# Kernel tuning notes

Measured on AMD Instinct MI355X. Metric: run time of the kernel, lower is better.

Reference implementation:

```python
import jax, jax.numpy as jnp
import numpy as np

B, N, K, D, F, H = 8, 512, 16, 256, 1024, 8


def _ln(x, g, b):
    m = jnp.mean(x, axis=-1, keepdims=True)
    v = jnp.var(x, axis=-1, keepdims=True)
    return (x - m) / jnp.sqrt(v + 1e-5) * g + b


def _mlp(x, W1, b1, W2, b2):
    return jax.nn.gelu(x @ W1 + b1, approximate=False) @ W2 + b2


def setup_inputs() -> dict:
    key = jax.random.key(0)
    ks = jax.random.split(key, 16)
    s = 0.02
    inp = {
        'x': jax.random.normal(ks[0], (N, B, D), jnp.float32),
        'e': jax.random.normal(ks[1], (B, N, K, D), jnp.float32),
        'edge_index': jax.random.randint(ks[2], (B, N, K), 0, N),
        'Wq': jax.random.normal(ks[3], (D, D), jnp.float32) * s,
        'bq': jnp.zeros((D,), jnp.float32),
        'Wk': jax.random.normal(ks[4], (D, D), jnp.float32) * s,
        'bk': jnp.zeros((D,), jnp.float32),
        'Wv': jax.random.normal(ks[5], (D, D), jnp.float32) * s,
        'bv': jnp.zeros((D,), jnp.float32),
        'Wo': jax.random.normal(ks[6], (D, D), jnp.float32) * s,
        'bo': jnp.zeros((D,), jnp.float32),
        'nW1': jax.random.normal(ks[7], (D, F), jnp.float32) * s,
        'nb1': jnp.zeros((F,), jnp.float32),
        'nW2': jax.random.normal(ks[8], (F, D), jnp.float32) * s,
        'nb2': jnp.zeros((D,), jnp.float32),
        'eW1': jax.random.normal(ks[9], (D, F), jnp.float32) * s,
        'eb1': jnp.zeros((F,), jnp.float32),
        'eW2': jax.random.normal(ks[10], (F, D), jnp.float32) * s,
        'eb2': jnp.zeros((D,), jnp.float32),
        'na_g': jnp.ones((D,), jnp.float32), 'na_b': jnp.zeros((D,), jnp.float32),
        'ea_g': jnp.ones((D,), jnp.float32), 'ea_b': jnp.zeros((D,), jnp.float32),
        'nf_g': jnp.ones((D,), jnp.float32), 'nf_b': jnp.zeros((D,), jnp.float32),
        'ef_g': jnp.ones((D,), jnp.float32), 'ef_b': jnp.zeros((D,), jnp.float32),
    }
    return inp


def reference(x, e, edge_index, Wq, bq, Wk, bk, Wv, bv, Wo, bo,
              nW1, nb1, nW2, nb2, eW1, eb1, eW2, eb2,
              na_g, na_b, ea_g, ea_b, nf_g, nf_b, ef_g, ef_b):
    n, b, d = x.shape
    hd = d // H
    xt = jnp.transpose(x, (1, 0, 2))  # (B, N, D) residual in batch-first layout
    bi = jnp.arange(b)[:, None, None]
    ni = jnp.arange(n)[None, :, None]

    # scatter edge features into dense additive attention bias (B, N, N)
    attn_bias = jnp.zeros((b, n, n), x.dtype).at[bi, ni, edge_index].set(e.mean(-1))

    def heads(t):  # (B,N,D) -> (B,H,N,hd)
        return t.reshape(b, n, H, hd).transpose(0, 2, 1, 3)

    q = heads(xt @ Wq + bq) * (hd ** -0.5)
    k = heads(xt @ Wk + bk)
    v = heads(xt @ Wv + bv)
    logits = jnp.einsum('bhnd,bhmd->bhnm', q, k) + attn_bias[:, None]
    attn = jax.nn.softmax(logits, axis=-1)  # (B,H,N,N)
    out = jnp.einsum('bhnm,bhmd->bhnd', attn, v)
    out = out.transpose(0, 2, 1, 3).reshape(b, n, d) @ Wo + bo

    xn = _ln(xt + out, na_g, na_b)  # (B,N,D)

    # edge update: gather attn weights and neighbor node features via edge_index
    weights = attn.mean(axis=1)  # (B,N,N) head-averaged
    w = weights[bi, edge_index, ni]  # (B,N,K): weights[b, edge_index[b,n,k], n]
    gathered = xt[jnp.arange(b)[:, None, None], edge_index]  # (B,N,K,D)
    e2 = _ln(e + w[..., None] * gathered, ea_g, ea_b)

    xn = _ln(xn + _mlp(xn, nW1, nb1, nW2, nb2), nf_g, nf_b)
    e2 = _ln(e2 + _mlp(e2, eW1, eb1, eW2, eb2), ef_g, ef_b)
    return jnp.transpose(xn, (1, 0, 2)), e2
```

## Files before the change

### kernel.cpp

```cpp
#include <hip/hip_runtime.h>
#include <hip/hip_bf16.h>
#include <hip/hip_fp8.h>
#include <math.h>

#define B_ 8
#define N_ 512
#define K_ 16
#define D_ 256
#define F_ 1024
#define H_ 8
#define HD_ 32
#define M_ (B_*N_)
#define R_ (B_*N_*K_)

typedef __bf16 bf16x8 __attribute__((ext_vector_type(8)));
typedef float  f32x4  __attribute__((ext_vector_type(4)));
typedef long   i64x2  __attribute__((ext_vector_type(2)));

__device__ inline short bf16s(float f) {
    __hip_bfloat16 h = __float2bfloat16(f);
    return *reinterpret_cast<short*>(&h);
}
__device__ inline float b2f(short s) {
    union { float f; unsigned u; } v; v.u = ((unsigned)(unsigned short)s) << 16; return v.f;
}
__device__ inline unsigned char f8e4m3(float f) {
    union { __hip_fp8_e4m3 h; unsigned char c; } u;
    u.h = __hip_fp8_e4m3(f);
    return u.c;
}
__device__ __forceinline__ float gelu_f(float x) {
    const float z = fabsf(x) * 0.70710678118654752f;
    const float t = __builtin_amdgcn_rcpf(1.f + 0.3275911f*z);
    const float p = t*(0.254829592f + t*(-0.284496736f + t*(1.421413741f
                  + t*(-1.453152027f + t*1.061405429f))));
    float er = 1.f - p*__expf(-z*z);
    er = (x >= 0.f) ? er : -er;
    return 0.5f*x*(1.f + er);
}
__device__ __forceinline__ int f8pos(int w, int row) {
    return ((((w >> 3) & 3) ^ (row & 3)) << 4) | ((w >> 5) << 3) | (w & 7);
}
__device__ __forceinline__ int hperm(int k) {
    return (k & ~63) | ((k & 15) << 2) | ((k >> 4) & 3);
}

__device__ __forceinline__ void gload16(const void* g, void* l) {
    __builtin_amdgcn_global_load_lds(
        (const __attribute__((address_space(1))) unsigned int*)g,
        (__attribute__((address_space(3))) unsigned int*)l, 16, 0, 0);
}

__global__ __launch_bounds__(256) void transposeAll(
        const float* __restrict__ Wq, const float* __restrict__ Wk,
        const float* __restrict__ Wv, const float* __restrict__ Wo,
        const float* __restrict__ nW1, const float* __restrict__ nW2,
        const float* __restrict__ eW1, const float* __restrict__ eW2,
        short* __restrict__ WqkvT, short* __restrict__ WoT,
        short* __restrict__ nW1T, short* __restrict__ nW2T,
        short* __restrict__ eW1T, unsigned char* __restrict__ eW2T8)
{
    const float* W; short* WT = nullptr; int Kk, Nn; float sc = 1.f;
    switch (blockIdx.z) {
        case 0: W=Wq;  WT=WqkvT;          Kk=256;  Nn=256;  sc=0.17677669529663687f; break;
        case 1: W=Wk;  WT=WqkvT+256*256;  Kk=256;  Nn=256;  break;
        case 2: W=Wv;  WT=WqkvT+512*256;  Kk=256;  Nn=256;  break;
        case 3: W=Wo;  WT=WoT;            Kk=256;  Nn=256;  break;
        case 4: W=nW1; WT=nW1T;           Kk=256;  Nn=1024; break;
        case 5: W=nW2; WT=nW2T;           Kk=1024; Nn=256;  break;
        case 6: W=eW1; WT=eW1T;           Kk=256;  Nn=1024; break;
        default:W=eW2;                    Kk=1024; Nn=256;  break;
    }
    const int bx = blockIdx.x, by = blockIdx.y;
    if (bx >= Nn/32 || by >= Kk/32) return;
    __shared__ float tile[32][33];
    int tx = threadIdx.x & 31, ty = threadIdx.x >> 5;
    #pragma unroll
    for (int j = 0; j < 4; ++j) {
        int k = by*32 + ty + j*8;
        tile[ty + j*8][tx] = W[(size_t)k*Nn + bx*32 + tx];
    }
    __syncthreads();
    if (blockIdx.z == 7) {
        #pragma unroll
        for (int j = 0; j < 4; ++j) {
            int n = bx*32 + ty + j*8;
            int kp = hperm(by*32 + tx);
            eW2T8[(size_t)n*1024 + (kp & ~63) + f8pos(kp & 63, n)] =
                f8e4m3(tile[tx][ty + j*8] * 64.f);
        }
    } else if (blockIdx.z == 5) {
        #pragma unroll
        for (int j = 0; j < 4; ++j) {
            int n = bx*32 + ty + j*8;
            WT[(size_t)n*1024 + hperm(by*32 + tx)] = bf16s(tile[tx][ty + j*8]);
        }
    } else {
        #pragma unroll
        for (int j = 0; j < 4; ++j) {
            int n = bx*32 + ty + j*8;
            WT[(size_t)n*Kk + by*32 + tx] = bf16s(tile[tx][ty + j*8] * sc);
        }
    }
}

__global__ __launch_bounds__(256) void build_bqkv(const float* __restrict__ bq,
        const float* __restrict__ bk, const float* __restrict__ bv,
        float* __restrict__ bqkv)
{
    int t = blockIdx.x*256 + threadIdx.x;
    if (t >= 768) return;
    float v = (t < 256) ? bq[t]*0.17677669529663687f
            : (t < 512) ? bk[t-256] : bv[t-512];
    bqkv[t] = v;
}

__global__ __launch_bounds__(256) void conv_x(const float* __restrict__ x,
        short* __restrict__ xtb)
{
    int row = blockIdx.x;
    int d = threadIdx.x;
    int b = row >> 9, n = row & 511;
    xtb[(size_t)row*D_ + d] = bf16s(x[((size_t)n*B_ + b)*D_ + d]);
}

__global__ __launch_bounds__(256) void edge_means(const float* __restrict__ e,
        float* __restrict__ means)
{
    long row = (long)blockIdx.x*4 + (threadIdx.x >> 6);
    int lane = threadIdx.x & 63;
    float4 v = ((const float4*)(e + row*D_))[lane];
    float s = v.x + v.y + v.z + v.w;
    for (int o = 1; o < 64; o <<= 1) s += __shfl_xor(s, o);
    if (lane == 0) means[row] = s * (1.f/D_);
}

__global__ __launch_bounds__(256) void bias_build(const int* __restrict__ ei,
        const float* __restrict__ means, float* __restrict__ biasb)
{
    const int r0 = blockIdx.x * 16;
    float4* bp4 = (float4*)(biasb + (size_t)r0*N_);
    #pragma unroll
    for (int i = threadIdx.x; i < 16*N_/4; i += 256)
        bp4[i] = make_float4(0.f, 0.f, 0.f, 0.f);
    __syncthreads();
    if (threadIdx.x < 16) {
        const int idx = r0 + threadIdx.x;
        const int* ep = ei + (size_t)idx*K_;
        const float* mp = means + (size_t)idx*K_;
        float* bp = biasb + (size_t)idx*N_;
        for (int k = 0; k < K_; ++k) bp[ep[k]] = mp[k];
    }
}

__global__ __launch_bounds__(256) void gemm_qkv(
        const short* __restrict__ A, const short* __restrict__ BT,
        const float* __restrict__ bias, short* __restrict__ Cb,
        short* __restrict__ vtb, int Kk)
{
    __shared__ __align__(16) short As[128*32];
    __shared__ __align__(16) short Bs[128*32];
    const int t = threadIdx.x;
    const int lane = t & 63;
    const int wave = t >> 6;
    const int wr = (wave >> 1) * 64;
    const int wc = (wave & 1) * 64;
    const int bm = blockIdx.x, bn = blockIdx.y;
    f32x4 acc[4][4] = {};
    const int srow = lane >> 2;
    const int sk   = (lane & 3) * 8;
    const int fr = lane & 15;
    const int fk = (lane >> 4) * 8;
    for (int k0 = 0; k0 < Kk; k0 += 32) {
        __syncthreads();
        #pragma unroll
        for (int i = 0; i < 2; ++i) {
            const int rb = wave*16 + i*64;
            gload16(A  + (size_t)(bm*128 + rb + srow)*Kk + k0 + sk, &As[rb*32]);
            gload16(BT + (size_t)(bn*128 + rb + srow)*Kk + k0 + sk, &Bs[rb*32]);
        }
        __syncthreads();
        bf16x8 af[4], bfr[4];
        #pragma unroll
        for (int i2 = 0; i2 < 4; ++i2)
            af[i2] = *(const bf16x8*)&As[(wr + i2*16 + fr)*32 + fk];
        #pragma unroll
        for (int n2 = 0; n2 < 4; ++n2)
            bfr[n2] = *(const bf16x8*)&Bs[(wc + n2*16 + fr)*32 + fk];
        #pragma unroll
        for (int i2 = 0; i2 < 4; ++i2)
            #pragma unroll
            for (int n2 = 0; n2 < 4; ++n2)
                acc[i2][n2] = __builtin_amdgcn_mfma_f32_16x16x32_bf16(
                        af[i2], bfr[n2], acc[i2][n2], 0, 0, 0);
    }
    const int fq4 = (lane >> 4) * 4;
    #pragma unroll
    for (int i2 = 0; i2 < 4; ++i2) {
        #pragma unroll
        for (int n2 = 0; n2 < 4; ++n2) {
            const int col = bn*128 + wc + n2*16 + fr;
            const float bv = bias[col];
            const int rowb = bm*128 + wr + i2*16 + fq4;
            if (col < 512) {
                #pragma unroll
                for (int r2 = 0; r2 < 4; ++r2)
                    Cb[(size_t)(rowb + r2)*512 + col] = bf16s(acc[i2][n2][r2] + bv);
            } else {
                const int b = rowb >> 9, n = rowb & 511;
                const int dv = col - 512, h = dv >> 5, dh = dv & 31;
                short4 s4;
                s4.x = bf16s(acc[i2][n2][0] + bv);
                s4.y = bf16s(acc[i2][n2][1] + bv);
                s4.z = bf16s(acc[i2][n2][2] + bv);
                s4.w = bf16s(acc[i2][n2][3] + bv);
                *(short4*)&vtb[((size_t)((b*H_ + h)*HD_ + dh))*512 + n] = s4;
            }
        }
    }
}

__global__ __launch_bounds__(512, 4) void gemm_gelu_f8(
        const short* __restrict__ A, const short* __restrict__ BT,
        const float* __restrict__ bias, unsigned char* __restrict__ C8, int Kk)
{
    __shared__ __align__(16) short As[2][128*32];
    __shared__ __align__(16) short Bs[2][256*32];
    const int t = threadIdx.x;
    const int lane = t & 63;
    const int wave = t >> 6;
    const int wrg = (wave >> 2) * 64;
    const int wc  = (wave & 3) * 64;
    const int bm = blockIdx.x, bn = blockIdx.y;
    f32x4 acc[4][4] = {};
    const int srow = lane >> 2;
    const int sk   = (lane & 3) * 8;
    const int fr = lane & 15;
    const int fk = (lane >> 4) * 8;
    auto stage = [&](int s, int k0) {
        {
            const int rb = wave*16;
            gload16(A + (size_t)(bm*128 + rb + srow)*Kk + k0 + sk, &As[s][rb*32]);
        }
        #pragma unroll
        for (int i = 0; i < 2; ++i) {
            const int rb = wave*16 + i*128;
            gload16(BT + (size_t)(bn*256 + rb + srow)*Kk + k0 + sk, &Bs[s][rb*32]);
        }
    };
    stage(0, 0);
    __syncthreads();
    int cur = 0;
    for (int k0 = 0; k0 < Kk; k0 += 32) {
        if (k0 + 32 < Kk) stage(cur ^ 1, k0 + 32);
        bf16x8 af[4], bfr[4];
        #pragma unroll
        for (int i2 = 0; i2 < 4; ++i2)
            af[i2] = *(const bf16x8*)&As[cur][(wrg + i2*16 + fr)*32 + fk];
        #pragma unroll
        for (int n2 = 0; n2 < 4; ++n2)
            bfr[n2] = *(const bf16x8*)&Bs[cur][(wc + n2*16 + fr)*32 + fk];
        #pragma unroll
        for (int i2 = 0; i2 < 4; ++i2)
            #pragma unroll
            for (int n2 = 0; n2 < 4; ++n2)
                acc[i2][n2] = __builtin_amdgcn_mfma_f32_16x16x32_bf16(
                        af[i2], bfr[n2], acc[i2][n2], 0, 0, 0);
        __syncthreads();
        cur ^= 1;
    }
    const int fq4 = (lane >> 4) * 4;
    const int chunk = (bn*4 + (wc >> 6)) * 64;
    #pragma unroll
    for (int i2 = 0; i2 < 4; ++i2) {
        #pragma unroll
        for (int r2 = 0; r2 < 4; ++r2) {
            const int row = bm*128 + wrg + i2*16 + fq4 + r2;
            float v[4];
            #pragma unroll
            for (int n2 = 0; n2 < 4; ++n2)
                v[n2] = gelu_f(acc[i2][n2][r2] + bias[bn*256 + wc + n2*16 + fr]);
            int word = __builtin_amdgcn_cvt_pk_fp8_f32(v[0]*16.f, v[1]*16.f, 0, false);
            word = __builtin_amdgcn_cvt_pk_fp8_f32(v[2]*16.f, v[3]*16.f, word, true);
            *(unsigned int*)(C8 + (size_t)row*1024 + chunk + f8pos(fr*4, row))
                = (unsigned int)word;
        }
    }
}

template<int MODE>
__global__ __launch_bounds__(256, 3) void gemm64(
        const short* __restrict__ A, const short* __restrict__ BT,
        const float* __restrict__ bias, const float* __restrict__ resf,
        const float* __restrict__ g, const float* __restrict__ bt,
        float* __restrict__ out, short* __restrict__ outb, int Kk)
{
    __shared__ __align__(16) short As[2][64*32];
    __shared__ __align__(16) short Bs[2][256*32];
    __shared__ float rs[64][4][2];
    __shared__ float mr[64][2];
    const int t = threadIdx.x;
    const int lane = t & 63;
    const int wave = t >> 6;
    const int wc = wave * 64;
    const int bm = blockIdx.x;
    const int Bbase = (MODE == 0) ? blockIdx.y * 256 : 0;
    f32x4 acc[4][4] = {};
    const int srow = lane >> 2;
    const int sk   = (lane & 3) * 8;
    const int fr = lane & 15;
    const int fk = (lane >> 4) * 8;
    auto stage = [&](int s, int k0) {
        {
            const int rb = wave*16;
            gload16(A + (size_t)(bm*64 + rb + srow)*Kk + k0 + sk, &As[s][rb*32]);
        }
        #pragma unroll
        for (int i = 0; i < 4; ++i) {
            const int rb = wave*16 + i*64;
            gload16(BT + (size_t)(Bbase + rb + srow)*Kk + k0 + sk, &Bs[s][rb*32]);
        }
    };
    stage(0, 0);
    __syncthreads();
    int cur = 0;
    for (int k0 = 0; k0 < Kk; k0 += 32) {
        if (k0 + 32 < Kk) stage(cur ^ 1, k0 + 32);
        bf16x8 af[4], bfr[4];
        #pragma unroll
        for (int i2 = 0; i2 < 4; ++i2)
            af[i2] = *(const bf16x8*)&As[cur][(i2*16 + fr)*32 + fk];
        #pragma unroll
        for (int n2 = 0; n2 < 4; ++n2)
            bfr[n2] = *(const bf16x8*)&Bs[cur][(wc + n2*16 + fr)*32 + fk];
        #pragma unroll
        for (int i2 = 0; i2 < 4; ++i2)
            #pragma unroll
            for (int n2 = 0; n2 < 4; ++n2)
                acc[i2][n2] = __builtin_amdgcn_mfma_f32_16x16x32_bf16(
                        af[i2], bfr[n2], acc[i2][n2], 0, 0, 0);
        __syncthreads();
        cur ^= 1;
    }
    const int fq4 = (lane >> 4) * 4;
    if constexpr (MODE == 0) {
        const int chunk = (blockIdx.y*4 + (wc >> 6)) * 64;
        #pragma unroll
        for (int i2 = 0; i2 < 4; ++i2) {
            #pragma unroll
            for (int r2 = 0; r2 < 4; ++r2) {
                const int row = bm*64 + i2*16 + fq4 + r2;
                float v[4];
                #pragma unroll
                for (int n2 = 0; n2 < 4; ++n2)
                    v[n2] = gelu_f(acc[i2][n2][r2]
                                   + bias[blockIdx.y*256 + wc + n2*16 + fr]);
                short4 s4;
                s4.x = bf16s(v[0]); s4.y = bf16s(v[1]);
                s4.z = bf16s(v[2]); s4.w = bf16s(v[3]);
                *(short4*)&outb[(size_t)row*1024 + chunk + fr*4] = s4;
            }
        }
        return;
    }
    float ps[4][4] = {}, pq[4][4] = {};
    #pragma unroll
    for (int i2 = 0; i2 < 4; ++i2) {
        #pragma unroll
        for (int n2 = 0; n2 < 4; ++n2) {
            const int c = wc + n2*16 + fr;
            const float bv = bias[c];
            #pragma unroll
            for (int r2 = 0; r2 < 4; ++r2) {
                const int row = i2*16 + fq4 + r2;
                const size_t grow = (size_t)bm*64 + row;
                float rv;
                if constexpr (MODE == 1) {
                    const int bb = (int)(grow >> 9), nn = (int)(grow & 511);
                    rv = resf[((size_t)nn*B_ + bb)*256 + c];
                } else {
                    rv = resf[grow*256 + c];
                }
                float v = acc[i2][n2][r2] + bv + rv;
                acc[i2][n2][r2] = v;
                ps[i2][r2] += v;
                pq[i2][r2] += v*v;
            }
        }
    }
    #pragma unroll
    for (int i2 = 0; i2 < 4; ++i2)
        #pragma unroll
        for (int r2 = 0; r2 < 4; ++r2)
            #pragma unroll
            for (int o = 1; o < 16; o <<= 1) {
                ps[i2][r2] += __shfl_xor(ps[i2][r2], o);
                pq[i2][r2] += __shfl_xor(pq[i2][r2], o);
            }
    if ((lane & 15) == 0) {
        #pragma unroll
        for (int i2 = 0; i2 < 4; ++i2)
            #pragma unroll
            for (int r2 = 0; r2 < 4; ++r2) {
                const int row = i2*16 + fq4 + r2;
                rs[row][wave][0] = ps[i2][r2];
                rs[row][wave][1] = pq[i2][r2];
            }
    }
    __syncthreads();
    if (t < 64) {
        float S = 0.f, Q = 0.f;
        #pragma unroll
        for (int w = 0; w < 4; ++w) { S += rs[t][w][0]; Q += rs[t][w][1]; }
        const float mean = S * (1.f/D_);
        mr[t][0] = mean;
        mr[t][1] = rsqrtf(Q * (1.f/D_) - mean*mean + 1e-5f);
    }
    __syncthreads();
    #pragma unroll
    for (int i2 = 0; i2 < 4; ++i2) {
        #pragma unroll
        for (int n2 = 0; n2 < 4; ++n2) {
            const int c = wc + n2*16 + fr;
            const float gv = g[c], bv2 = bt[c];
            #pragma unroll
            for (int r2 = 0; r2 < 4; ++r2) {
                const int row = i2*16 + fq4 + r2;
                const size_t grow = (size_t)bm*64 + row;
                const float o = (acc[i2][n2][r2] - mr[row][0])*mr[row][1]*gv + bv2;
                if constexpr (MODE == 1) {
                    out[grow*256 + c] = o;
                    outb[grow*256 + c] = bf16s(o);
                } else {
                    const int bb = (int)(grow >> 9), nn = (int)(grow & 511);
                    out[((size_t)nn*B_ + bb)*D_ + c] = o;
                }
            }
        }
    }
}

__global__ __launch_bounds__(512, 4) void gemm_ln2f8(
        const unsigned char* __restrict__ A, const unsigned char* __restrict__ BT,
        const float* __restrict__ bias, const short* __restrict__ resb,
        const float* __restrict__ g, const float* __restrict__ bt,
        float* __restrict__ out)
{
    __shared__ __align__(16) unsigned char As[2][128*64];
    __shared__ __align__(16) unsigned char Bs[2][256*64];
    __shared__ float rs[128][4][2];
    __shared__ float mr[128][2];
    const int t = threadIdx.x;
    const int lane = t & 63;
    const int wave = t >> 6;
    const int wrg = (wave >> 2) * 64;
    const int wc  = (wave & 3) * 64;
    const int bm = blockIdx.x;
    f32x4 acc[4][4] = {};
    const int srow = lane >> 2;
    const int skb  = (lane & 3) * 16;
    const int fr = lane & 15;
    const int q16 = (lane >> 4);
    auto stage = [&](int s, int k0) {
        {
            const int rb = wave*16;
            gload16(A + (size_t)(bm*128 + rb + srow)*1024 + k0 + skb, &As[s][rb*64]);
        }
        #pragma unroll
        for (int i = 0; i < 2; ++i) {
            const int rb = wave*16 + i*128;
            gload16(BT + (size_t)(rb + srow)*1024 + k0 + skb, &Bs[s][rb*64]);
        }
    };
    stage(0, 0);
    __syncthreads();
    int cur = 0;
    for (int k0 = 0; k0 < 1024; k0 += 64) {
        if (k0 + 64 < 1024) stage(cur ^ 1, k0 + 64);
        long a8[2][4], b8[2][4];
        #pragma unroll
        for (int i2 = 0; i2 < 4; ++i2) {
            const int ar = wrg + i2*16 + fr;
            const i64x2 av = *(const i64x2*)&As[cur][ar*64 + ((q16 ^ (ar & 3)) << 4)];
            a8[0][i2] = av[0]; a8[1][i2] = av[1];
        }
        #pragma unroll
        for (int n2 = 0; n2 < 4; ++n2) {
            const int br = wc + n2*16 + fr;
            const i64x2 bv = *(const i64x2*)&Bs[cur][br*64 + ((q16 ^ (br & 3)) << 4)];
            b8[0][n2] = bv[0]; b8[1][n2] = bv[1];
        }
        #pragma unroll
        for (int s = 0; s < 2; ++s)
            #pragma unroll
            for (int i2 = 0; i2 < 4; ++i2)
                #pragma unroll
                for (int n2 = 0; n2 < 4; ++n2)
                    acc[i2][n2] = __builtin_amdgcn_mfma_f32_16x16x32_fp8_fp8(
                            a8[s][i2], b8[s][n2], acc[i2][n2], 0, 0, 0);
        __syncthreads();
        cur ^= 1;
    }
    const int fq4 = (lane >> 4) * 4;
    float ps[4][4] = {}, pq[4][4] = {};
    #pragma unroll
    for (int i2 = 0; i2 < 4; ++i2) {
        #pragma unroll
        for (int n2 = 0; n2 < 4; ++n2) {
            const int c = wc + n2*16 + fr;
            const float bv = bias[c];
            #pragma unroll
            for (int r2 = 0; r2 < 4; ++r2) {
                const int row = wrg + i2*16 + fq4 + r2;
                const size_t grow = (size_t)bm*128 + row;
                float v = acc[i2][n2][r2]*(1.f/1024.f) + bv + b2f(resb[grow*256 + c]);
                acc[i2][n2][r2] = v;
                ps[i2][r2] += v;
                pq[i2][r2] += v*v;
            }
        }
    }
    #pragma unroll
    for (int i2 = 0; i2 < 4; ++i2)
        #pragma unroll
        for (int r2 = 0; r2 < 4; ++r2)
            #pragma unroll
            for (int o = 1; o < 16; o <<= 1) {
                ps[i2][r2] += __shfl_xor(ps[i2][r2], o);
                pq[i2][r2] += __shfl_xor(pq[i2][r2], o);
            }
    if ((lane & 15) == 0) {
        #pragma unroll
        for (int i2 = 0; i2 < 4; ++i2)
            #pragma unroll
            for (int r2 = 0; r2 < 4; ++r2) {
                const int row = wrg + i2*16 + fq4 + r2;
                rs[row][wave & 3][0] = ps[i2][r2];
                rs[row][wave & 3][1] = pq[i2][r2];
            }
    }
    __syncthreads();
    if (t < 128) {
        float S = 0.f, Q = 0.f;
        #pragma unroll
        for (int w = 0; w < 4; ++w) { S += rs[t][w][0]; Q += rs[t][w][1]; }
        const float mean = S * (1.f/D_);
        mr[t][0] = mean;
        mr[t][1] = rsqrtf(Q * (1.f/D_) - mean*mean + 1e-5f);
    }
    __syncthreads();
    #pragma unroll
    for (int i2 = 0; i2 < 4; ++i2) {
        #pragma unroll
        for (int n2 = 0; n2 < 4; ++n2) {
            const int c = wc + n2*16 + fr;
            const float gv = g[c], bv2 = bt[c];
            #pragma unroll
            for (int r2 = 0; r2 < 4; ++r2) {
                const int row = wrg + i2*16 + fq4 + r2;
                const size_t grow = (size_t)bm*128 + row;
                out[grow*256 + c] = (acc[i2][n2][r2] - mr[row][0])*mr[row][1]*gv + bv2;
            }
        }
    }
}

__global__ __launch_bounds__(256) void attn_fused(const short* __restrict__ qkb,
        const short* __restrict__ vtb, const float* __restrict__ biasb,
        float* __restrict__ rowsum, short* __restrict__ actx)
{
    __shared__ __align__(16) short Qs[128*32];
    __shared__ __align__(16) short Ks[128*32];
    __shared__ __align__(16) short Vs[32*128];
    __shared__ __align__(16) short Ps[128*128];
    const int it = blockIdx.x, bh = blockIdx.y;
    const int b = bh >> 3, h = bh & 7;
    const int t = threadIdx.x;
    const int lane = t & 63;
    const int wave = t >> 6;
    const int wr0 = wave * 32;
    const int srow = lane >> 2;
    const int sk   = (lane & 3) * 8;
    const int srow8 = lane >> 4;
    const int ck16  = lane & 15;
    const int fr = lane & 15;
    const int fk = (lane >> 4) * 8;
    const int fq4 = (lane >> 4) * 4;
    const int I0 = it * 128;
    #pragma unroll
    for (int i = 0; i < 2; ++i) {
        const int rb = wave*16 + i*64;
        gload16(qkb + (size_t)(b*N_ + I0 + rb + srow)*512 + h*HD_ + sk, &Qs[rb*32]);
    }
    float rsum[2][4] = {};
    f32x4 apv[2][2] = {};
    const float LOG2E = 1.4426950408889634f;
    for (int jt = 0; jt < 4; ++jt) {
        const int J0 = jt * 128;
        __syncthreads();
        #pragma unroll
        for (int i = 0; i < 2; ++i) {
            const int rb = wave*16 + i*64;
            gload16(qkb + (size_t)(b*N_ + J0 + rb + srow)*512 + 256 + h*HD_ + sk, &Ks[rb*32]);
        }
        #pragma unroll
        for (int i = 0; i < 2; ++i) {
            const int db = wave*8 + i*4;
            const int dh = db + srow8;
            gload16(vtb + ((size_t)bh*HD_ + dh)*512 + J0 + ((ck16 ^ (dh & 7)) * 8),
                    &Vs[db*128]);
        }
        __syncthreads();
        bf16x8 aq[2], kf8[8];
        #pragma unroll
        for (int i2 = 0; i2 < 2; ++i2)
            aq[i2] = *(const bf16x8*)&Qs[(wr0 + i2*16 + fr)*32 + fk];
        #pragma unroll
        for (int n2 = 0; n2 < 8; ++n2)
            kf8[n2] = *(const bf16x8*)&Ks[(n2*16 + fr)*32 + fk];
        #pragma unroll
        for (int i2 = 0; i2 < 2; ++i2) {
            #pragma unroll
            for (int n2 = 0; n2 < 8; ++n2) {
                f32x4 z = {0.f, 0.f, 0.f, 0.f};
                f32x4 s = __builtin_amdgcn_mfma_f32_16x16x32_bf16(aq[i2], kf8[n2], z, 0, 0, 0);
                const int jg = J0 + n2*16 + fr;
                #pragma unroll
                for (int r2 = 0; r2 < 4; ++r2) {
                    const int rloc = wr0 + i2*16 + fq4 + r2;
                    const float l = s[r2] + biasb[((size_t)b*N_ + I0 + rloc)*N_ + jg];
                    const float p = exp2f(fminf(l, 80.f) * LOG2E);
                    rsum[i2][r2] += p;
                    int idx = rloc*128 + n2*16 + fr;
                    idx ^= (rloc & 7) << 3;
                    Ps[idx] = bf16s(p);
                }
            }
        }
        __syncthreads();
        #pragma unroll
        for (int ks = 0; ks < 4; ++ks) {
            bf16x8 ap[2], bv[2];
            #pragma unroll
            for (int i2 = 0; i2 < 2; ++i2) {
                const int r = wr0 + i2*16 + fr;
                int idx = r*128 + ks*32 + fk;
                idx ^= (r & 7) << 3;
                ap[i2] = *(const bf16x8*)&Ps[idx];
            }
            #pragma unroll
            for (int n2 = 0; n2 < 2; ++n2) {
                const int dh = n2*16 + fr;
                const int q = lane >> 4;
                const int slot = (ks*4 + q) ^ (dh & 7);
                bv[n2] = *(const bf16x8*)&Vs[dh*128 + slot*8];
            }
            #pragma unroll
            for (int i2 = 0; i2 < 2; ++i2)
                #pragma unroll
                for (int n2 = 0; n2 < 2; ++n2)
                    apv[i2][n2] = __builtin_amdgcn_mfma_f32_16x16x32_bf16(
                            ap[i2], bv[n2], apv[i2][n2], 0, 0, 0);
        }
    }
    #pragma unroll
    for (int i2 = 0; i2 < 2; ++i2)
        #pragma unroll
        for (int r2 = 0; r2 < 4; ++r2)
            #pragma unroll
            for (int o = 1; o < 16; o <<= 1)
                rsum[i2][r2] += __shfl_xor(rsum[i2][r2], o);
    #pragma unroll
    for (int i2 = 0; i2 < 2; ++i2) {
        #pragma unroll
        for (int r2 = 0; r2 < 4; ++r2) {
            const int row = wr0 + i2*16 + fq4 + r2;
            if (fr == 0)
                rowsum[(size_t)bh*N_ + I0 + row] = rsum[i2][r2];
            const float inv = 1.f / rsum[i2][r2];
            #pragma unroll
            for (int n2 = 0; n2 < 2; ++n2)
                actx[((size_t)b*N_ + I0 + row)*D_ + h*HD_ + n2*16 + fr]
                    = bf16s(apv[i2][n2][r2] * inv);
        }
    }
}

__device__ inline void ln_core(float v[4], int lane, const float* __restrict__ g,
        const float* __restrict__ bt, float out[4])
{
    float s  = v[0] + v[1] + v[2] + v[3];
    float sq = v[0]*v[0] + v[1]*v[1] + v[2]*v[2] + v[3]*v[3];
    for (int o = 1; o < 64; o <<= 1) { s += __shfl_xor(s, o); sq += __shfl_xor(sq, o); }
    float mean = s * (1.f/D_);
    float rstd = rsqrtf(sq * (1.f/D_) - mean*mean + 1e-5f);
    const float4 gv = *(const float4*)(g  + lane*4);
    const float4 bv = *(const float4*)(bt + lane*4);
    out[0] = (v[0]-mean)*rstd*gv.x + bv.x;
    out[1] = (v[1]-mean)*rstd*gv.y + bv.y;
    out[2] = (v[2]-mean)*rstd*gv.z + bv.z;
    out[3] = (v[3]-mean)*rstd*gv.w + bv.w;
}

__global__ __launch_bounds__(256) void edge_update(const float* __restrict__ e,
        const float* __restrict__ x, const int* __restrict__ ei,
        const short* __restrict__ qkb, const float* __restrict__ biasb,
        const float* __restrict__ rowsum, const float* __restrict__ g,
        const float* __restrict__ bt, short* __restrict__ e2b)
{
    long row = (long)blockIdx.x*4 + (threadIdx.x >> 6);
    int lane = threadIdx.x & 63;
    long bi = row >> 4;
    long b = bi / N_; int i = (int)(bi % N_);
    int ej = ei[row];
    const short4 q4 = *(const short4*)(qkb + ((size_t)b*N_ + ej)*512 + lane*4);
    const short4 k4 = *(const short4*)(qkb + ((size_t)b*N_ + i)*512 + 256 + lane*4);
    float dot = b2f(q4.x)*b2f(k4.x) + b2f(q4.y)*b2f(k4.y)
              + b2f(q4.z)*b2f(k4.z) + b2f(q4.w)*b2f(k4.w);
    dot += __shfl_xor(dot, 1); dot += __shfl_xor(dot, 2); dot += __shfl_xor(dot, 4);
    const int h = lane >> 3;
    const float l = dot + biasb[((size_t)b*N_ + ej)*N_ + i];
    float p = exp2f(fminf(l, 80.f) * 1.4426950408889634f)
            / rowsum[((size_t)b*H_ + h)*N_ + ej];
    p += __shfl_xor(p, 8); p += __shfl_xor(p, 16); p += __shfl_xor(p, 32);
    const float w = p * (1.f/H_);
    const float4 ev = *(const float4*)(e + row*D_ + lane*4);
    const float4 xv = *(const float4*)(x + ((size_t)ej*B_ + b)*D_ + lane*4);
    float v[4] = {ev.x + w*xv.x, ev.y + w*xv.y, ev.z + w*xv.z, ev.w + w*xv.w};
    float o[4];
    ln_core(v, lane, g, bt, o);
    short4 s4; s4.x = bf16s(o[0]); s4.y = bf16s(o[1]); s4.z = bf16s(o[2]); s4.w = bf16s(o[3]);
    *(short4*)(e2b + row*D_ + lane*4) = s4;
}

extern "C" void kernel_launch(void* const* d_in, const int* in_sizes, int n_in,
                              void* d_out, int out_size, void* d_ws, size_t ws_size,
                              hipStream_t stream)
{
    (void)in_sizes; (void)n_in; (void)out_size; (void)ws_size;
    const float* x    = (const float*)d_in[0];
    const float* e    = (const float*)d_in[1];
    const int*   ei   = (const int*)d_in[2];
    const float* Wq   = (const float*)d_in[3];
    const float* bq   = (const float*)d_in[4];
    const float* Wk   = (const float*)d_in[5];
    const float* bk   = (const float*)d_in[6];
    const float* Wv   = (const float*)d_in[7];
    const float* bv   = (const float*)d_in[8];
    const float* Wo   = (const float*)d_in[9];
    const float* bo   = (const float*)d_in[10];
    const float* nW1  = (const float*)d_in[11];
    const float* nb1  = (const float*)d_in[12];
    const float* nW2  = (const float*)d_in[13];
    const float* nb2  = (const float*)d_in[14];
    const float* eW1  = (const float*)d_in[15];
    const float* eb1  = (const float*)d_in[16];
    const float* eW2  = (const float*)d_in[17];
    const float* eb2  = (const float*)d_in[18];
    const float* na_g = (const float*)d_in[19];
    const float* na_b = (const float*)d_in[20];
    const float* ea_g = (const float*)d_in[21];
    const float* ea_b = (const float*)d_in[22];
    const float* nf_g = (const float*)d_in[23];
    const float* nf_b = (const float*)d_in[24];
    const float* ef_g = (const float*)d_in[25];
    const float* ef_b = (const float*)d_in[26];

    float* out1 = (float*)d_out;
    float* e2f  = out1 + (size_t)N_*B_*D_;

    char* wp = (char*)d_ws;
    auto alloc = [&](size_t bytes) -> char* {
        char* p = wp; wp += (bytes + 255) & ~(size_t)255; return p;
    };
    short* WqkvT  = (short*)alloc((size_t)768*D_*2);
    float* bqkv   = (float*)alloc(768*4);
    short* WoT    = (short*)alloc((size_t)D_*D_*2);
    short* nW1T   = (short*)alloc((size_t)F_*D_*2);
    short* nW2T   = (short*)alloc((size_t)D_*F_*2);
    short* eW1T   = (short*)alloc((size_t)F_*D_*2);
    unsigned char* eW2T8 = (unsigned char*)alloc((size_t)D_*F_);
    float* rowsum = (float*)alloc((size_t)B_*H_*N_*4);
    short* e2b    = (short*)alloc((size_t)R_*D_*2);
    char* ov = wp;
    auto allocA = [&](size_t bytes) -> char* {
        char* p = ov; ov += (bytes + 255) & ~(size_t)255; return p;
    };
    short* xtb    = (short*)allocA((size_t)M_*D_*2);
    float* means  = (float*)allocA((size_t)R_*4);
    float* biasb  = (float*)allocA((size_t)B_*N_*N_*4);
    short* qkb    = (short*)allocA((size_t)M_*512*2);
    short* vtb    = (short*)allocA((size_t)B_*H_*HD_*N_*2);
    short* actx   = (short*)allocA((size_t)M_*D_*2);
    float* xn     = (float*)allocA((size_t)M_*D_*4);
    short* xnb    = (short*)allocA((size_t)M_*D_*2);
    short* nhid   = (short*)allocA((size_t)M_*F_*2);
    unsigned char* ehid8 = (unsigned char*)wp;

    transposeAll<<<dim3(32, 32, 8), 256, 0, stream>>>(Wq, Wk, Wv, Wo,
            nW1, nW2, eW1, eW2, WqkvT, WoT, nW1T, nW2T, eW1T, eW2T8);
    build_bqkv<<<3, 256, 0, stream>>>(bq, bk, bv, bqkv);
    conv_x<<<M_, 256, 0, stream>>>(x, xtb);

    edge_means<<<R_/4, 256, 0, stream>>>(e, means);
    bias_build<<<M_/16, 256, 0, stream>>>(ei, means, biasb);

    gemm_qkv<<<dim3(M_/128, 768/128), 256, 0, stream>>>(
            xtb, WqkvT, bqkv, qkb, vtb, D_);

    attn_fused<<<dim3(N_/128, B_*H_), 256, 0, stream>>>(qkb, vtb, biasb, rowsum, actx);

    gemm64<1><<<M_/64, 256, 0, stream>>>(
            actx, WoT, bo, x, na_g, na_b, xn, xnb, D_);
    gemm64<0><<<dim3(M_/64, F_/256), 256, 0, stream>>>(
            xnb, nW1T, nb1, nullptr, nullptr, nullptr, nullptr, nhid, D_);
    gemm64<2><<<M_/64, 256, 0, stream>>>(
            nhid, nW2T, nb2, xn, nf_g, nf_b, out1, nullptr, F_);

    edge_update<<<R_/4, 256, 0, stream>>>(e, x, ei, qkb, biasb, rowsum,
            ea_g, ea_b, e2b);
    gemm_gelu_f8<<<dim3(R_/128, F_/256), 512, 0, stream>>>(
            e2b, eW1T, eb1, ehid8, D_);
    gemm_ln2f8<<<R_/128, 512, 0, stream>>>(
            ehid8, eW2T8, eb2, e2b, ef_g, ef_b, e2f);
}
```

Baseline: 308.9 us.

## Deepen GEMM prefetch to two stages in flight with explicit vmcnt waits

Restructures the double-buffered K loops of the bf16 GEMM (gelu/fp8 output) and the fp8 GEMM (residual+LN epilogue) so two global-to-LDS stages are issued before the loop. Each iteration reads fragments, waits for LDS reads, barriers, then refills the freed buffer two steps ahead. Partial vmcnt(3) waits replace the full __syncthreads drain, so loads can overlap MFMA work. The loops are fully unrolled with hardcoded trip counts (8 and 16), and correctness depends on each stage issuing exactly three loads.

Measured after the change: 305.6 us, median of 2. Within noise of the previous version (-1.1%).

```diff
diff --git a/kernel.cpp b/kernel.cpp
--- a/kernel.cpp
+++ b/kernel.cpp
@@ -249,10 +249,13 @@
         }
     };
     stage(0, 0);
-    __syncthreads();
-    int cur = 0;
-    for (int k0 = 0; k0 < Kk; k0 += 32) {
-        if (k0 + 32 < Kk) stage(cur ^ 1, k0 + 32);
+    stage(1, 32);
+    asm volatile("s_waitcnt vmcnt(3)" ::: "memory");
+    __builtin_amdgcn_sched_barrier(0);
+    __builtin_amdgcn_s_barrier();
+    #pragma unroll
+    for (int tt = 0; tt < 8; ++tt) {
+        const int cur = tt & 1;
         bf16x8 af[4], bfr[4];
         #pragma unroll
         for (int i2 = 0; i2 < 4; ++i2)
@@ -260,14 +263,20 @@
         #pragma unroll
         for (int n2 = 0; n2 < 4; ++n2)
             bfr[n2] = *(const bf16x8*)&Bs[cur][(wc + n2*16 + fr)*32 + fk];
+        asm volatile("s_waitcnt lgkmcnt(0)" ::: "memory");
+        __builtin_amdgcn_sched_barrier(0);
+        __builtin_amdgcn_s_barrier();
+        if (tt + 2 < 8) stage(cur, (tt + 2) * 32);
         #pragma unroll
         for (int i2 = 0; i2 < 4; ++i2)
             #pragma unroll
             for (int n2 = 0; n2 < 4; ++n2)
                 acc[i2][n2] = __builtin_amdgcn_mfma_f32_16x16x32_bf16(
                         af[i2], bfr[n2], acc[i2][n2], 0, 0, 0);
-        __syncthreads();
-        cur ^= 1;
+        if (tt + 2 < 8) { asm volatile("s_waitcnt vmcnt(3)" ::: "memory"); }
+        else            { asm volatile("s_waitcnt vmcnt(0)" ::: "memory"); }
+        __builtin_amdgcn_sched_barrier(0);
+        __builtin_amdgcn_s_barrier();
     }
     const int fq4 = (lane >> 4) * 4;
     const int chunk = (bn*4 + (wc >> 6)) * 64;
@@ -473,10 +482,13 @@
         }
     };
     stage(0, 0);
-    __syncthreads();
-    int cur = 0;
-    for (int k0 = 0; k0 < 1024; k0 += 64) {
-        if (k0 + 64 < 1024) stage(cur ^ 1, k0 + 64);
+    stage(1, 64);
+    asm volatile("s_waitcnt vmcnt(3)" ::: "memory");
+    __builtin_amdgcn_sched_barrier(0);
+    __builtin_amdgcn_s_barrier();
+    #pragma unroll
+    for (int tt = 0; tt < 16; ++tt) {
+        const int cur = tt & 1;
         long a8[2][4], b8[2][4];
         #pragma unroll
         for (int i2 = 0; i2 < 4; ++i2) {
@@ -490,6 +502,10 @@
             const i64x2 bv = *(const i64x2*)&Bs[cur][br*64 + ((q16 ^ (br & 3)) << 4)];
             b8[0][n2] = bv[0]; b8[1][n2] = bv[1];
         }
+        asm volatile("s_waitcnt lgkmcnt(0)" ::: "memory");
+        __builtin_amdgcn_sched_barrier(0);
+        __builtin_amdgcn_s_barrier();
+        if (tt + 2 < 16) stage(cur, (tt + 2) * 64);
         #pragma unroll
         for (int s = 0; s < 2; ++s)
             #pragma unroll
@@ -498,8 +514,10 @@
                 for (int n2 = 0; n2 < 4; ++n2)
                     acc[i2][n2] = __builtin_amdgcn_mfma_f32_16x16x32_fp8_fp8(
                             a8[s][i2], b8[s][n2], acc[i2][n2], 0, 0, 0);
-        __syncthreads();
-        cur ^= 1;
+        if (tt + 2 < 16) { asm volatile("s_waitcnt vmcnt(3)" ::: "memory"); }
+        else             { asm volatile("s_waitcnt vmcnt(0)" ::: "memory"); }
+        __builtin_amdgcn_sched_barrier(0);
+        __builtin_amdgcn_s_barrier();
     }
     const int fq4 = (lane >> 4) * 4;
     float ps[4][4] = {}, pq[4][4] = {};
```
